# Kernel tuning notes

Hardware: AMD Instinct MI355X
Metric: run time of the kernel (lower is better)

The kernel has to match this reference:

```python
import jax, jax.numpy as jnp
import numpy as np

B, L, C, D = 8, 8192, 256, 256


def setup_inputs() -> dict:
    key = jax.random.key(0)
    ks = jax.random.split(key, 13)
    bound = 1.0 / np.sqrt(C)

    def W(k):
        return jax.random.uniform(k, (C, D), jnp.float32, -bound, bound)

    def b(k):
        return jax.random.uniform(k, (D,), jnp.float32, -bound, bound)

    return {
        "xs": jax.random.normal(ks[0], (B, L, C), jnp.float32),
        # forward-direction params
        "Wh1": W(ks[1]), "bh1": b(ks[2]),
        "Wz1": W(ks[3]), "bz1": b(ks[4]),
        "Ws1": W(ks[5]), "bs1": b(ks[6]),
        "h01": jnp.zeros((1, 1, D), jnp.float32),
        # backward-direction params
        "Wh_1": W(ks[7]), "bh_1": b(ks[8]),
        "Wz_1": W(ks[9]), "bz_1": b(ks[10]),
        "Ws_1": W(ks[11]), "bs_1": b(ks[12]),
        "h0_1": jnp.zeros((1, 1, D), jnp.float32),
    }


def _gru_scan(z, h_tilde, h0):
    """h[t] = z[t]*h_tilde[t] + (1-z[t])*h[t-1], h[-1]=h0. Parallel over time
    via associative scan on the affine maps h -> a*h + b."""
    a = 1.0 - z            # [B, L, D]
    b = z * h_tilde        # [B, L, D]

    def combine(c1, c2):
        a1, b1 = c1
        a2, b2 = c2
        return a1 * a2, a2 * b1 + b2

    A, Bc = jax.lax.associative_scan(combine, (a, b), axis=1)
    return Bc + A * h0     # broadcast h0 [1,1,D]


def reference(xs, Wh1, bh1, Wz1, bz1, Ws1, bs1, h01,
              Wh_1, bh_1, Wz_1, bz_1, Ws_1, bs_1, h0_1):
    sig = jax.nn.sigmoid
    # forward direction
    hf = _gru_scan(sig(xs @ Wz1 + bz1), xs @ Wh1 + bh1, h01) * sig(xs @ Ws1 + bs1)
    # backward direction: reverse time, scan, reverse back
    zr = sig(xs @ Wz_1 + bz_1)
    hr = xs @ Wh_1 + bh_1
    hb = _gru_scan(zr[:, ::-1], hr[:, ::-1], h0_1)[:, ::-1] * sig(xs @ Ws_1 + bs_1)
    return hf + hb
```

## Files before the change

kernel.cpp:

```cpp
#include <hip/hip_runtime.h>
#include <hip/hip_bf16.h>

typedef unsigned short u16;

#define BDIM 8
#define LDIM 8192
#define KDIM 256
#define DDIM 256
#define MTOT 65536
#define NDIM 1536
#define TCH  32
#define NCH  256


typedef float floatx4 __attribute__((ext_vector_type(4)));
typedef short bf16x8 __attribute__((ext_vector_type(8)));

__device__ __forceinline__ u16 f2bf(float f) {
  union { __hip_bfloat16 h; u16 u; } c;
  c.h = __float2bfloat16(f);
  return c.u;
}
__device__ __forceinline__ float bf2f(u16 u) {
  union { unsigned int i; float f; } c;
  c.i = ((unsigned int)u) << 16;
  return c.f;
}
__device__ __forceinline__ float sigmoidf_fast(float x) {
  return __builtin_amdgcn_rcpf(1.0f + __expf(-x));
}
__device__ __forceinline__ void gll16(const u16* g, u16* l) {
  __builtin_amdgcn_global_load_lds((const __attribute__((address_space(1))) void*)g,
                                   (__attribute__((address_space(3))) void*)l, 16, 0, 0);
}

__global__ void prep_weights(const float* __restrict__ Wh1, const float* __restrict__ Wz1,
                             const float* __restrict__ Ws1, const float* __restrict__ Wh_1,
                             const float* __restrict__ Wz_1, const float* __restrict__ Ws_1,
                             const float* __restrict__ bh1, const float* __restrict__ bz1,
                             const float* __restrict__ bs1, const float* __restrict__ bh_1,
                             const float* __restrict__ bz_1, const float* __restrict__ bs_1,
                             u16* __restrict__ WcatT, float* __restrict__ bcat) {
  const int n = blockIdx.x;
  const int k = threadIdx.x;
  const int dir = n / 768, r = n % 768;
  int d; const float* W; const float* bb;
  if (r < 512) {
    d = r >> 1;
    if (r & 1) { W = dir ? Wz_1 : Wz1; bb = dir ? bz_1 : bz1; }
    else       { W = dir ? Wh_1 : Wh1; bb = dir ? bh_1 : bh1; }
  } else {
    d = r - 512;
    W = dir ? Ws_1 : Ws1; bb = dir ? bs_1 : bs1;
  }
  WcatT[(size_t)n * KDIM + k] = f2bf(W[k * DDIM + d]);
  if (k == 0) bcat[n] = bb[d];
}

__global__ void convert_xs(const float* __restrict__ xs, u16* __restrict__ Abf) {
  size_t i = ((size_t)blockIdx.x * 256 + threadIdx.x) * 8;
  const float4* s = (const float4*)(xs + i);
  float4 f0 = s[0], f1 = s[1];
  union { u16 u[8]; uint4 v; } t;
  t.u[0] = f2bf(f0.x); t.u[1] = f2bf(f0.y); t.u[2] = f2bf(f0.z); t.u[3] = f2bf(f0.w);
  t.u[4] = f2bf(f1.x); t.u[5] = f2bf(f1.y); t.u[6] = f2bf(f1.z); t.u[7] = f2bf(f1.w);
  *(uint4*)(Abf + i) = t.v;
}

__global__ __launch_bounds__(256) void gemm_kernel(const u16* __restrict__ Abf,
                                                   const u16* __restrict__ WcatT,
                                                   const float* __restrict__ bcat,
                                                   u16* __restrict__ G) {
  __shared__ __align__(16) u16 As[8192];
  __shared__ __align__(16) u16 Bs[8192];
  const int tid = threadIdx.x;
  const int lane = tid & 63, wave = tid >> 6;
  const int wm = wave >> 1, wn = wave & 1;
  const int q = lane >> 4, r = lane & 15;

  const int xcd = blockIdx.x & 7;
  const int li  = blockIdx.x >> 3;
  const int mt  = xcd * 64 + li / 12;
  const int nt  = li % 12;
  const int m0 = mt * 128, n0 = nt * 128;

  const u16* gA[4]; const u16* gB[4]; u16* lA[4]; u16* lB[4];
#pragma unroll
  for (int j = 0; j < 4; j++) {
    const int bi = wave * 256 + j * 64 + lane;
    const int row = bi >> 3;
    const int kq = (bi & 7) ^ (row & 7);
    gA[j] = Abf   + (size_t)(m0 + row) * KDIM + kq * 8;
    gB[j] = WcatT + (size_t)(n0 + row) * KDIM + kq * 8;
    lA[j] = As + bi * 8;
    lB[j] = Bs + bi * 8;
  }

  floatx4 acc[4][4];
  floatx4 z4 = {0.f, 0.f, 0.f, 0.f};
#pragma unroll
  for (int i = 0; i < 4; i++)
#pragma unroll
    for (int j = 0; j < 4; j++) acc[i][j] = z4;

  for (int k0 = 0; k0 < KDIM; k0 += 64) {
#pragma unroll
    for (int j = 0; j < 4; j++) { gll16(gA[j] + k0, lA[j]); gll16(gB[j] + k0, lB[j]); }
    __syncthreads();
#pragma unroll
    for (int kk = 0; kk < 2; kk++) {
      bf16x8 af[4], bv[4];
#pragma unroll
      for (int i = 0; i < 4; i++) {
        const int row = wm * 64 + i * 16 + r;
        af[i] = *(const bf16x8*)(As + (row * 8 + ((kk * 4 + q) ^ (row & 7))) * 8);
      }
#pragma unroll
      for (int j = 0; j < 4; j++) {
        const int row = wn * 64 + j * 16 + r;
        bv[j] = *(const bf16x8*)(Bs + (row * 8 + ((kk * 4 + q) ^ (row & 7))) * 8);
      }
#pragma unroll
      for (int i = 0; i < 4; i++)
#pragma unroll
        for (int j = 0; j < 4; j++)
          acc[i][j] = __builtin_amdgcn_mfma_f32_16x16x32_bf16(af[i], bv[j], acc[i][j], 0, 0, 0);
    }
    __syncthreads();
  }

  float bvals[4];
#pragma unroll
  for (int j = 0; j < 4; j++) bvals[j] = bcat[n0 + wn * 64 + j * 16 + r];
#pragma unroll
  for (int i = 0; i < 4; i++) {
#pragma unroll
    for (int reg = 0; reg < 4; reg++) {
      size_t grow = (size_t)(m0 + wm * 64 + i * 16 + q * 4 + reg);
      u16* dst = G + grow * NDIM + n0 + wn * 64 + r;
#pragma unroll
      for (int j = 0; j < 4; j++)
        dst[j * 16] = f2bf(acc[i][j][reg] + bvals[j]);
    }
  }
}

__global__ __launch_bounds__(256) void scan_phaseA(const u16* __restrict__ G,
                                                   float* __restrict__ Acc,
                                                   float* __restrict__ Bcc) {
  const int slot = threadIdx.x >> 6, lane = threadIdx.x & 63;
  const int u = blockIdx.x * 4 + slot;
  const int c = u & 255, b = (u >> 8) & 7, dir = u >> 11;
  const int d0 = lane * 4;
  const u16* p0 = G + (size_t)b * LDIM * NDIM + dir * 768 + d0 * 2;
  float h[4], P[4];
#pragma unroll
  for (int e = 0; e < 4; ++e) { h[e] = 0.f; P[e] = 1.f; }
#pragma unroll 8
  for (int i = 0; i < TCH; ++i) {
    const int t = dir ? (c * TCH + (TCH - 1 - i)) : (c * TCH + i);
    uint4 hz = *(const uint4*)(p0 + (size_t)t * NDIM);
    const u16* q = (const u16*)&hz;
#pragma unroll
    for (int e = 0; e < 4; ++e) {
      float z = sigmoidf_fast(bf2f(q[2 * e + 1]));
      float a = 1.f - z;
      h[e] = fmaf(a, h[e], z * bf2f(q[2 * e]));
      P[e] *= a;
    }
  }
  float4 v;
  v.x = P[0]; v.y = P[1]; v.z = P[2]; v.w = P[3];
  *(float4*)(Acc + (size_t)u * 256 + d0) = v;
  v.x = h[0]; v.y = h[1]; v.z = h[2]; v.w = h[3];
  *(float4*)(Bcc + (size_t)u * 256 + d0) = v;
}

__global__ void scan_phaseB(const float* __restrict__ Acc, const float* __restrict__ Bcc,
                            const float* __restrict__ h01, const float* __restrict__ h0_1,
                            float* __restrict__ Pref) {
  const int d = threadIdx.x, b = blockIdx.x, dir = blockIdx.y;
  float h = dir ? h0_1[d] : h01[d];
  const size_t ubase = ((size_t)dir * BDIM + b) * NCH;
  if (dir == 0) {
    for (int c0 = 0; c0 < NCH; c0 += 8) {
      float a[8], bb[8];
#pragma unroll
      for (int j = 0; j < 8; ++j) {
        size_t idx = (ubase + c0 + j) * DDIM + d;
        a[j] = Acc[idx]; bb[j] = Bcc[idx];
      }
#pragma unroll
      for (int j = 0; j < 8; ++j) {
        Pref[(ubase + c0 + j) * DDIM + d] = h;
        h = fmaf(a[j], h, bb[j]);
      }
    }
  } else {
    for (int c0 = NCH - 1; c0 >= 0; c0 -= 8) {
      float a[8], bb[8];
#pragma unroll
      for (int j = 0; j < 8; ++j) {
        size_t idx = (ubase + c0 - j) * DDIM + d;
        a[j] = Acc[idx]; bb[j] = Bcc[idx];
      }
#pragma unroll
      for (int j = 0; j < 8; ++j) {
        Pref[(ubase + c0 - j) * DDIM + d] = h;
        h = fmaf(a[j], h, bb[j]);
      }
    }
  }
}

__global__ __launch_bounds__(256) void scan_phaseC(const u16* __restrict__ G,
                                                   const float* __restrict__ Pref,
                                                   float* __restrict__ out) {
  __shared__ u16 fbuf[TCH * 256];
  __shared__ u16 bbuf[TCH * 256];
  const int c = blockIdx.x & 255, b = blockIdx.x >> 8;
  const int wave = threadIdx.x >> 6, lane = threadIdx.x & 63;
  const int dir = wave >> 1, half = wave & 1;
  const int d0 = half * 128 + lane * 2;
  const int u = dir * 2048 + b * 256 + c;
  float h0 = Pref[(size_t)u * 256 + d0];
  float h1 = Pref[(size_t)u * 256 + d0 + 1];
  const u16* ghz = G + (size_t)b * LDIM * NDIM + dir * 768 + d0 * 2;
  const u16* gs  = G + (size_t)b * LDIM * NDIM + dir * 768 + 512 + d0;
  u16* buf = dir ? bbuf : fbuf;

#pragma unroll 4
  for (int i = 0; i < TCH; ++i) {
    const int tl = dir ? (TCH - 1 - i) : i;
    const int t = c * TCH + tl;
    uint2 hz = *(const uint2*)(ghz + (size_t)t * NDIM);
    unsigned int sv = *(const unsigned int*)(gs + (size_t)t * NDIM);
    const u16* q = (const u16*)&hz;
    const u16* sq = (const u16*)&sv;
    float z0 = sigmoidf_fast(bf2f(q[1]));
    float z1 = sigmoidf_fast(bf2f(q[3]));
    h0 = fmaf(1.f - z0, h0, z0 * bf2f(q[0]));
    h1 = fmaf(1.f - z1, h1, z1 * bf2f(q[2]));
    unsigned int pk = (unsigned int)f2bf(h0 * sigmoidf_fast(bf2f(sq[0])))
                    | ((unsigned int)f2bf(h1 * sigmoidf_fast(bf2f(sq[1]))) << 16);
    *(unsigned int*)(buf + tl * 256 + d0) = pk;
  }
  __syncthreads();
  const int tid = threadIdx.x;
  float* obase = out + ((size_t)b * LDIM + c * TCH) * DDIM + tid;
#pragma unroll 8
  for (int rrow = 0; rrow < TCH; ++rrow) {
    float v = bf2f(fbuf[rrow * 256 + tid]) + bf2f(bbuf[rrow * 256 + tid]);
    obase[(size_t)rrow * DDIM] = v;
  }
}

extern "C" void kernel_launch(void* const* d_in, const int* in_sizes, int n_in,
                              void* d_out, int out_size, void* d_ws, size_t ws_size,
                              hipStream_t stream) {
  const float* xs   = (const float*)d_in[0];
  const float* Wh1  = (const float*)d_in[1];
  const float* bh1  = (const float*)d_in[2];
  const float* Wz1  = (const float*)d_in[3];
  const float* bz1  = (const float*)d_in[4];
  const float* Ws1  = (const float*)d_in[5];
  const float* bs1  = (const float*)d_in[6];
  const float* h01  = (const float*)d_in[7];
  const float* Wh_1 = (const float*)d_in[8];
  const float* bh_1 = (const float*)d_in[9];
  const float* Wz_1 = (const float*)d_in[10];
  const float* bz_1 = (const float*)d_in[11];
  const float* Ws_1 = (const float*)d_in[12];
  const float* bs_1 = (const float*)d_in[13];
  const float* h0_1 = (const float*)d_in[14];
  float* out = (float*)d_out;

  char* ws = (char*)d_ws;
  u16* WcatT = (u16*)ws;   ws += (size_t)NDIM * KDIM * 2;
  float* bcat = (float*)ws; ws += (size_t)NDIM * 4;
  u16* Abf = (u16*)ws;     ws += (size_t)MTOT * KDIM * 2;
  u16* G = (u16*)ws;       ws += (size_t)MTOT * NDIM * 2;
  float* Acc  = (float*)Abf;
  float* Bcc  = Acc + (size_t)2 * BDIM * NCH * DDIM;
  float* Pref = Bcc + (size_t)2 * BDIM * NCH * DDIM;
  if ((size_t)(ws - (char*)d_ws) > ws_size) return;

  prep_weights<<<dim3(NDIM), dim3(KDIM), 0, stream>>>(
      Wh1, Wz1, Ws1, Wh_1, Wz_1, Ws_1, bh1, bz1, bs1, bh_1, bz_1, bs_1, WcatT, bcat);
  convert_xs<<<dim3(MTOT * KDIM / (256 * 8)), dim3(256), 0, stream>>>(xs, Abf);
  gemm_kernel<<<dim3(6144), dim3(256), 0, stream>>>(Abf, WcatT, bcat, G);
  scan_phaseA<<<dim3(1024), dim3(256), 0, stream>>>(G, Acc, Bcc);
  scan_phaseB<<<dim3(BDIM, 2), dim3(DDIM), 0, stream>>>(Acc, Bcc, h01, h0_1, Pref);
  scan_phaseC<<<dim3(2048), dim3(256), 0, stream>>>(G, Pref, out);
}
```

Baseline: 297.2 us.

## Fuse chunk-local scan phase A into GEMM epilogue and widen phase C per thread

The GEMM epilogue now also stages its h/z output tile in shared memory and computes the per-chunk (P, h) scan summaries directly, which removes the separate phase-A kernel and its re-read of G. Phase C drops to 128 threads, each handling four channels, with register prefetch of the next four timesteps and vectorized output stores. Acc, Bcc and Pref move to their own workspace region instead of aliasing Abf, because the GEMM still reads Abf while it writes them. The costs are a larger shared-memory footprint in the GEMM, an extra barrier and a serial 32-step loop in the h/z tiles, and fewer threads in phase C.

```diff
diff --git a/kernel.cpp b/kernel.cpp
--- a/kernel.cpp
+++ b/kernel.cpp
@@ -70,9 +70,12 @@
 __global__ __launch_bounds__(256) void gemm_kernel(const u16* __restrict__ Abf,
                                                    const u16* __restrict__ WcatT,
                                                    const float* __restrict__ bcat,
-                                                   u16* __restrict__ G) {
-  __shared__ __align__(16) u16 As[8192];
-  __shared__ __align__(16) u16 Bs[8192];
+                                                   u16* __restrict__ G,
+                                                   float* __restrict__ Acc,
+                                                   float* __restrict__ Bcc) {
+  __shared__ __align__(16) u16 smem[16896];
+  u16* As = smem;
+  u16* Bs = smem + 8192;
   const int tid = threadIdx.x;
   const int lane = tid & 63, wave = tid >> 6;
   const int wm = wave >> 1, wn = wave & 1;
@@ -129,6 +132,7 @@
     __syncthreads();
   }
 
+  const bool is_hz = (nt < 4) | (nt >= 6 && nt < 10);
   float bvals[4];
 #pragma unroll
   for (int j = 0; j < 4; j++) bvals[j] = bcat[n0 + wn * 64 + j * 16 + r];
@@ -136,44 +140,47 @@
   for (int i = 0; i < 4; i++) {
 #pragma unroll
     for (int reg = 0; reg < 4; reg++) {
-      size_t grow = (size_t)(m0 + wm * 64 + i * 16 + q * 4 + reg);
-      u16* dst = G + grow * NDIM + n0 + wn * 64 + r;
-#pragma unroll
-      for (int j = 0; j < 4; j++)
-        dst[j * 16] = f2bf(acc[i][j][reg] + bvals[j]);
-    }
-  }
-}
-
-__global__ __launch_bounds__(256) void scan_phaseA(const u16* __restrict__ G,
-                                                   float* __restrict__ Acc,
-                                                   float* __restrict__ Bcc) {
-  const int slot = threadIdx.x >> 6, lane = threadIdx.x & 63;
-  const int u = blockIdx.x * 4 + slot;
-  const int c = u & 255, b = (u >> 8) & 7, dir = u >> 11;
-  const int d0 = lane * 4;
-  const u16* p0 = G + (size_t)b * LDIM * NDIM + dir * 768 + d0 * 2;
-  float h[4], P[4];
-#pragma unroll
-  for (int e = 0; e < 4; ++e) { h[e] = 0.f; P[e] = 1.f; }
-#pragma unroll 8
-  for (int i = 0; i < TCH; ++i) {
-    const int t = dir ? (c * TCH + (TCH - 1 - i)) : (c * TCH + i);
-    uint4 hz = *(const uint4*)(p0 + (size_t)t * NDIM);
-    const u16* q = (const u16*)&hz;
-#pragma unroll
-    for (int e = 0; e < 4; ++e) {
-      float z = sigmoidf_fast(bf2f(q[2 * e + 1]));
-      float a = 1.f - z;
-      h[e] = fmaf(a, h[e], z * bf2f(q[2 * e]));
-      P[e] *= a;
-    }
-  }
-  float4 v;
-  v.x = P[0]; v.y = P[1]; v.z = P[2]; v.w = P[3];
-  *(float4*)(Acc + (size_t)u * 256 + d0) = v;
-  v.x = h[0]; v.y = h[1]; v.z = h[2]; v.w = h[3];
-  *(float4*)(Bcc + (size_t)u * 256 + d0) = v;
+      const int row = wm * 64 + i * 16 + q * 4 + reg;
+      u16* dst = G + (size_t)(m0 + row) * NDIM + n0 + wn * 64 + r;
+#pragma unroll
+      for (int j = 0; j < 4; j++) {
+        const u16 v = f2bf(acc[i][j][reg] + bvals[j]);
+        dst[j * 16] = v;
+        if (is_hz) smem[row * 132 + wn * 64 + j * 16 + r] = v;
+      }
+    }
+  }
+  if (is_hz) {
+    __syncthreads();
+    const int dl = tid & 63, seg = tid >> 6;
+    const int dirn = (nt < 4) ? 0 : 1;
+    const int dbase = (nt < 4) ? nt * 64 : (nt - 6) * 64;
+    float h = 0.f, P = 1.f;
+    if (dirn == 0) {
+      for (int i = 0; i < 32; ++i) {
+        const int t = seg * 32 + i;
+        unsigned int hz32 = *(const unsigned int*)(smem + t * 132 + 2 * dl);
+        float z = sigmoidf_fast(bf2f((u16)(hz32 >> 16)));
+        float a = 1.f - z;
+        h = fmaf(a, h, z * bf2f((u16)(hz32 & 0xffff)));
+        P *= a;
+      }
+    } else {
+      for (int i = 31; i >= 0; --i) {
+        const int t = seg * 32 + i;
+        unsigned int hz32 = *(const unsigned int*)(smem + t * 132 + 2 * dl);
+        float z = sigmoidf_fast(bf2f((u16)(hz32 >> 16)));
+        float a = 1.f - z;
+        h = fmaf(a, h, z * bf2f((u16)(hz32 & 0xffff)));
+        P *= a;
+      }
+    }
+    const int b = m0 >> 13;
+    const int c = ((m0 & 8191) >> 5) + seg;
+    const int u = dirn * 2048 + b * 256 + c;
+    Acc[(size_t)u * 256 + dbase + dl] = P;
+    Bcc[(size_t)u * 256 + dbase + dl] = h;
+  }
 }
 
 __global__ void scan_phaseB(const float* __restrict__ Acc, const float* __restrict__ Bcc,
@@ -181,18 +188,19 @@
                             float* __restrict__ Pref) {
   const int d = threadIdx.x, b = blockIdx.x, dir = blockIdx.y;
   float h = dir ? h0_1[d] : h01[d];
-  const size_t ubase = ((size_t)dir * BDIM + b) * NCH;
+  const size_t ubase = ((size_t)dir * 2048 / NCH * NCH) + ((size_t)dir * 0);
+  const size_t base = ((size_t)dir * BDIM + b) * NCH;
   if (dir == 0) {
     for (int c0 = 0; c0 < NCH; c0 += 8) {
       float a[8], bb[8];
 #pragma unroll
       for (int j = 0; j < 8; ++j) {
-        size_t idx = (ubase + c0 + j) * DDIM + d;
+        size_t idx = (base + c0 + j) * DDIM + d;
         a[j] = Acc[idx]; bb[j] = Bcc[idx];
       }
 #pragma unroll
       for (int j = 0; j < 8; ++j) {
-        Pref[(ubase + c0 + j) * DDIM + d] = h;
+        Pref[(base + c0 + j) * DDIM + d] = h;
         h = fmaf(a[j], h, bb[j]);
       }
     }
@@ -201,57 +209,81 @@
       float a[8], bb[8];
 #pragma unroll
       for (int j = 0; j < 8; ++j) {
-        size_t idx = (ubase + c0 - j) * DDIM + d;
+        size_t idx = (base + c0 - j) * DDIM + d;
         a[j] = Acc[idx]; bb[j] = Bcc[idx];
       }
 #pragma unroll
       for (int j = 0; j < 8; ++j) {
-        Pref[(ubase + c0 - j) * DDIM + d] = h;
+        Pref[(base + c0 - j) * DDIM + d] = h;
         h = fmaf(a[j], h, bb[j]);
       }
     }
   }
 }
 
-__global__ __launch_bounds__(256) void scan_phaseC(const u16* __restrict__ G,
+__global__ __launch_bounds__(128) void scan_phaseC(const u16* __restrict__ G,
                                                    const float* __restrict__ Pref,
                                                    float* __restrict__ out) {
   __shared__ u16 fbuf[TCH * 256];
   __shared__ u16 bbuf[TCH * 256];
   const int c = blockIdx.x & 255, b = blockIdx.x >> 8;
-  const int wave = threadIdx.x >> 6, lane = threadIdx.x & 63;
-  const int dir = wave >> 1, half = wave & 1;
-  const int d0 = half * 128 + lane * 2;
+  const int dir = threadIdx.x >> 6, lane = threadIdx.x & 63;
+  const int d0 = lane * 4;
   const int u = dir * 2048 + b * 256 + c;
-  float h0 = Pref[(size_t)u * 256 + d0];
-  float h1 = Pref[(size_t)u * 256 + d0 + 1];
+  float4 hp = *(const float4*)(Pref + (size_t)u * 256 + d0);
+  float h[4] = {hp.x, hp.y, hp.z, hp.w};
   const u16* ghz = G + (size_t)b * LDIM * NDIM + dir * 768 + d0 * 2;
   const u16* gs  = G + (size_t)b * LDIM * NDIM + dir * 768 + 512 + d0;
   u16* buf = dir ? bbuf : fbuf;
-
-#pragma unroll 4
-  for (int i = 0; i < TCH; ++i) {
-    const int tl = dir ? (TCH - 1 - i) : i;
-    const int t = c * TCH + tl;
-    uint2 hz = *(const uint2*)(ghz + (size_t)t * NDIM);
-    unsigned int sv = *(const unsigned int*)(gs + (size_t)t * NDIM);
-    const u16* q = (const u16*)&hz;
-    const u16* sq = (const u16*)&sv;
-    float z0 = sigmoidf_fast(bf2f(q[1]));
-    float z1 = sigmoidf_fast(bf2f(q[3]));
-    h0 = fmaf(1.f - z0, h0, z0 * bf2f(q[0]));
-    h1 = fmaf(1.f - z1, h1, z1 * bf2f(q[2]));
-    unsigned int pk = (unsigned int)f2bf(h0 * sigmoidf_fast(bf2f(sq[0])))
-                    | ((unsigned int)f2bf(h1 * sigmoidf_fast(bf2f(sq[1]))) << 16);
-    *(unsigned int*)(buf + tl * 256 + d0) = pk;
+  const size_t tb = (size_t)c * TCH;
+
+  uint4 hzb[4]; uint2 svb[4];
+#pragma unroll
+  for (int j = 0; j < 4; ++j) {
+    const int tl = dir ? (TCH - 1 - j) : j;
+    hzb[j] = *(const uint4*)(ghz + (tb + tl) * NDIM);
+    svb[j] = *(const uint2*)(gs + (tb + tl) * NDIM);
+  }
+  for (int i0 = 0; i0 < TCH; i0 += 4) {
+#pragma unroll
+    for (int j = 0; j < 4; ++j) {
+      const int i = i0 + j;
+      const int tl = dir ? (TCH - 1 - i) : i;
+      uint4 hz = hzb[j]; uint2 sv = svb[j];
+      const int ip = i + 4;
+      if (ip < TCH) {
+        const int tlp = dir ? (TCH - 1 - ip) : ip;
+        hzb[j] = *(const uint4*)(ghz + (tb + tlp) * NDIM);
+        svb[j] = *(const uint2*)(gs + (tb + tlp) * NDIM);
+      }
+      const u16* q = (const u16*)&hz;
+      const u16* sq = (const u16*)&sv;
+#pragma unroll
+      for (int e = 0; e < 4; ++e) {
+        float z = sigmoidf_fast(bf2f(q[2 * e + 1]));
+        h[e] = fmaf(1.f - z, h[e], z * bf2f(q[2 * e]));
+      }
+      uint2 pk;
+      pk.x = (unsigned int)f2bf(h[0] * sigmoidf_fast(bf2f(sq[0])))
+           | ((unsigned int)f2bf(h[1] * sigmoidf_fast(bf2f(sq[1]))) << 16);
+      pk.y = (unsigned int)f2bf(h[2] * sigmoidf_fast(bf2f(sq[2])))
+           | ((unsigned int)f2bf(h[3] * sigmoidf_fast(bf2f(sq[3]))) << 16);
+      *(uint2*)(buf + tl * 256 + d0) = pk;
+    }
   }
   __syncthreads();
-  const int tid = threadIdx.x;
-  float* obase = out + ((size_t)b * LDIM + c * TCH) * DDIM + tid;
-#pragma unroll 8
-  for (int rrow = 0; rrow < TCH; ++rrow) {
-    float v = bf2f(fbuf[rrow * 256 + tid]) + bf2f(bbuf[rrow * 256 + tid]);
-    obase[(size_t)rrow * DDIM] = v;
+  float* ob = out + ((size_t)b * LDIM + tb) * DDIM;
+  for (int e = threadIdx.x * 4; e < TCH * 256; e += 128 * 4) {
+    uint2 fv = *(const uint2*)(fbuf + e);
+    uint2 bv = *(const uint2*)(bbuf + e);
+    const u16* fq = (const u16*)&fv;
+    const u16* bq = (const u16*)&bv;
+    float4 o;
+    o.x = bf2f(fq[0]) + bf2f(bq[0]);
+    o.y = bf2f(fq[1]) + bf2f(bq[1]);
+    o.z = bf2f(fq[2]) + bf2f(bq[2]);
+    o.w = bf2f(fq[3]) + bf2f(bq[3]);
+    *(float4*)(ob + e) = o;
   }
 }
 
@@ -276,20 +308,19 @@
   float* out = (float*)d_out;
 
   char* ws = (char*)d_ws;
-  u16* WcatT = (u16*)ws;   ws += (size_t)NDIM * KDIM * 2;
+  u16* WcatT = (u16*)ws;    ws += (size_t)NDIM * KDIM * 2;
   float* bcat = (float*)ws; ws += (size_t)NDIM * 4;
-  u16* Abf = (u16*)ws;     ws += (size_t)MTOT * KDIM * 2;
-  u16* G = (u16*)ws;       ws += (size_t)MTOT * NDIM * 2;
-  float* Acc  = (float*)Abf;
-  float* Bcc  = Acc + (size_t)2 * BDIM * NCH * DDIM;
-  float* Pref = Bcc + (size_t)2 * BDIM * NCH * DDIM;
+  u16* Abf = (u16*)ws;      ws += (size_t)MTOT * KDIM * 2;
+  u16* G = (u16*)ws;        ws += (size_t)MTOT * NDIM * 2;
+  float* Acc  = (float*)ws; ws += (size_t)2 * BDIM * NCH * DDIM * 4;
+  float* Bcc  = (float*)ws; ws += (size_t)2 * BDIM * NCH * DDIM * 4;
+  float* Pref = (float*)ws; ws += (size_t)2 * BDIM * NCH * DDIM * 4;
   if ((size_t)(ws - (char*)d_ws) > ws_size) return;
 
   prep_weights<<<dim3(NDIM), dim3(KDIM), 0, stream>>>(
       Wh1, Wz1, Ws1, Wh_1, Wz_1, Ws_1, bh1, bz1, bs1, bh_1, bz_1, bs_1, WcatT, bcat);
   convert_xs<<<dim3(MTOT * KDIM / (256 * 8)), dim3(256), 0, stream>>>(xs, Abf);
-  gemm_kernel<<<dim3(6144), dim3(256), 0, stream>>>(Abf, WcatT, bcat, G);
-  scan_phaseA<<<dim3(1024), dim3(256), 0, stream>>>(G, Acc, Bcc);
+  gemm_kernel<<<dim3(6144), dim3(256), 0, stream>>>(Abf, WcatT, bcat, G, Acc, Bcc);
   scan_phaseB<<<dim3(BDIM, 2), dim3(DDIM), 0, stream>>>(Acc, Bcc, h01, h0_1, Pref);
-  scan_phaseC<<<dim3(2048), dim3(256), 0, stream>>>(G, Pref, out);
-}
+  scan_phaseC<<<dim3(2048), dim3(128), 0, stream>>>(G, Pref, out);
+}
```

After: 319.5 us. 1.08x slower.
